# Performance work log

Hardware: AMD Instinct MI355X
Metric: run time of the kernel (lower is better)

Reference implementation:

```python
import jax, jax.numpy as jnp
import numpy as np

B, S, E, H = 2, 2048, 1024, 16
D = E // H
LN_EPS = 1e-5
NORM_EPS = 1e-12  # F.normalize clamp_min


def setup_inputs() -> dict:
    key = jax.random.key(0)
    ks = jax.random.split(key, 4)
    x = jax.random.normal(ks[0], (B, S, E), dtype=jnp.float32)
    qkv_w = jax.random.normal(ks[1], (3 * E, E), dtype=jnp.float32) * 0.02
    qkv_b = jnp.zeros((3 * E,), dtype=jnp.float32)
    out_w = jax.random.normal(ks[2], (E, E), dtype=jnp.float32) * 0.02
    out_b = jnp.zeros((E,), dtype=jnp.float32)
    ln_w = jnp.ones((E,), dtype=jnp.float32)
    ln_b = jnp.zeros((E,), dtype=jnp.float32)
    qknorm_scale = jnp.asarray(E ** -0.5, dtype=jnp.float32)
    # RotaryEmbedding buffer: inv_freq interleaved (emb[::2] = emb[1::2] = base**(-arange(0,E,2)/E))
    base_freq = 10000.0 ** (-(np.arange(0, E, 2).astype(np.float32) / E))
    emb = np.empty((E,), dtype=np.float32)
    emb[::2] = base_freq
    emb[1::2] = base_freq
    inv_freq = jnp.asarray(emb)
    return {"x": x, "ln_w": ln_w, "ln_b": ln_b, "qkv_w": qkv_w, "qkv_b": qkv_b,
            "qknorm_scale": qknorm_scale, "out_w": out_w, "out_b": out_b, "inv_freq": inv_freq}


def _rotate(t, sin, cos):
    # Faithful to source: x1 = even idx (excluding last), x2 = odd idx; cat(-x2, x1)
    x1 = t[..., :-1:2]
    x2 = t[..., 1::2]
    t_rot = jnp.concatenate((-x2, x1), axis=-1)
    return t * cos + t_rot * sin


def _l2norm(t):
    n = jnp.sqrt(jnp.sum(t * t, axis=-1, keepdims=True))
    return t / jnp.maximum(n, NORM_EPS)


def reference(x, ln_w, ln_b, qkv_w, qkv_b, qknorm_scale, out_w, out_b, inv_freq):
    # --- prenorm (LayerNorm, eps=1e-5) ---
    mu = jnp.mean(x, axis=-1, keepdims=True)
    var = jnp.mean((x - mu) ** 2, axis=-1, keepdims=True)
    xn = (x - mu) / jnp.sqrt(var + LN_EPS) * ln_w + ln_b
    # --- QKV projection ---
    qkv = xn @ qkv_w.T + qkv_b  # [B,S,3E]
    q, k, v = jnp.split(qkv, 3, axis=-1)
    # --- rotary (source uses scalar seq*inv_freq, not per-position) ---
    seq = q.shape[1]
    sin = jnp.sin(seq * inv_freq)
    cos = jnp.cos(seq * inv_freq)
    q = _rotate(q, sin, cos)
    k = _rotate(k, sin, cos)
    # --- split heads: [B,S,E] -> [B,H,S,D] ---
    split = lambda t: t.reshape(B, seq, H, D).transpose(0, 2, 1, 3)
    q, k, v = split(q), split(k), split(v)
    # --- qknorm ---
    q = _l2norm(q) * qknorm_scale
    k = _l2norm(k) * qknorm_scale
    # --- scaled dot product with causal mask ---
    aw = jnp.einsum('bhqd,bhkd->bhqk', q, k)  # [B,H,S,S]
    causal = jnp.tril(jnp.ones((seq, seq), dtype=bool))
    aw = jnp.where(causal, aw, jnp.finfo(aw.dtype).min)
    aw = jax.nn.softmax(aw, axis=-1)
    attn = jnp.einsum('bhqk,bhkd->bhqd', aw, v)
    # --- merge heads + out proj ---
    attn = attn.transpose(0, 2, 1, 3).reshape(B, seq, E)
    return attn @ out_w.T + out_b
```

## Files before the change

kernel.cpp:

```cpp
#include <hip/hip_runtime.h>

typedef unsigned short u16;
typedef __attribute__((ext_vector_type(8))) short bf16x8;
typedef __attribute__((ext_vector_type(4))) float f32x4;

#define SS 2048
#define EE 1024
#define HH 16
#define DD 64

__device__ __forceinline__ float b2f(u16 u) {
  union { unsigned int i; float f; } v; v.i = ((unsigned int)u) << 16; return v.f;
}
__device__ __forceinline__ u16 f2b(float f) {
  union { float f; unsigned int i; } v; v.f = f;
  unsigned int i = v.i;
  return (u16)((i + 0x7FFFu + ((i >> 16) & 1u)) >> 16);
}

#define GLD16(g, l)                                                         \
  __builtin_amdgcn_global_load_lds(                                         \
      (const __attribute__((address_space(1))) unsigned int*)(g),           \
      (__attribute__((address_space(3))) unsigned int*)(l), 16, 0, 0)

__global__ __launch_bounds__(256) void k_cvt(const float* __restrict__ src,
                                             u16* __restrict__ dst) {
  const int i = blockIdx.x * 256 + threadIdx.x;
  float4 v = ((const float4*)src)[i];
  ushort4 o;
  o.x = f2b(v.x); o.y = f2b(v.y); o.z = f2b(v.z); o.w = f2b(v.w);
  ((ushort4*)dst)[i] = o;
}

__global__ __launch_bounds__(256) void k_trig(const float* __restrict__ inv_freq,
                                              float2* __restrict__ cs) {
  const int i = blockIdx.x * 256 + threadIdx.x;
  float th = 2048.0f * inv_freq[i];
  cs[i] = make_float2(cosf(th), sinf(th));
}

__global__ __launch_bounds__(256) void k_ln(const float* __restrict__ x,
                                            const float* __restrict__ lw,
                                            const float* __restrict__ lb,
                                            u16* __restrict__ xn) {
  const int row = blockIdx.x, t = threadIdx.x;
  float4 v = ((const float4*)(x + (size_t)row * EE))[t];
  float f0 = v.x, f1 = v.y, f2 = v.z, f3 = v.w;
  float s = f0 + f1 + f2 + f3;
  float ss = f0 * f0 + f1 * f1 + f2 * f2 + f3 * f3;
  for (int o = 1; o < 64; o <<= 1) { s += __shfl_xor(s, o); ss += __shfl_xor(ss, o); }
  __shared__ float red[8];
  int w = t >> 6;
  if ((t & 63) == 0) { red[w] = s; red[4 + w] = ss; }
  __syncthreads();
  s = red[0] + red[1] + red[2] + red[3];
  ss = red[4] + red[5] + red[6] + red[7];
  float mu = s * (1.0f / 1024.0f);
  float var = ss * (1.0f / 1024.0f) - mu * mu;
  float rstd = rsqrtf(var + 1e-5f);
  float4 wv = ((const float4*)lw)[t];
  float4 bv = ((const float4*)lb)[t];
  ushort4 o;
  o.x = f2b((f0 - mu) * rstd * wv.x + bv.x);
  o.y = f2b((f1 - mu) * rstd * wv.y + bv.y);
  o.z = f2b((f2 - mu) * rstd * wv.z + bv.z);
  o.w = f2b((f3 - mu) * rstd * wv.w + bv.w);
  ((ushort4*)(xn + (size_t)row * EE))[t] = o;
}

template <typename OutT>
__device__ __forceinline__ void gemm_body(const u16* __restrict__ A,
                                          const u16* __restrict__ W,
                                          const float* __restrict__ bias,
                                          OutT* __restrict__ C,
                                          int M, int N, int K) {
  __shared__ __align__(16) u16 As[128 * 32];
  __shared__ __align__(16) u16 Ws[128 * 32];
  const int t = threadIdx.x;
  const int m0 = blockIdx.y * 128, n0 = blockIdx.x * 128;
  const int lane = t & 63, w = t >> 6, quad = lane >> 4, l15 = lane & 15;
  const int wm = (w & 1) * 64, wn = (w >> 1) * 64;

  f32x4 zero4 = {0.f, 0.f, 0.f, 0.f};
  f32x4 acc[4][4];
  for (int mi = 0; mi < 4; mi++)
    for (int ni = 0; ni < 4; ni++) acc[mi][ni] = zero4;

  const u16* Ag = A + (size_t)(m0 + (t >> 2)) * K + (t & 3) * 8;
  const u16* Wg = W + (size_t)(n0 + (t >> 2)) * K + (t & 3) * 8;
  const size_t rowskip = (size_t)64 * K;

  for (int k0 = 0; k0 < K; k0 += 32) {
    GLD16(Ag + k0, As + t * 8);
    GLD16(Ag + rowskip + k0, As + 2048 + t * 8);
    GLD16(Wg + k0, Ws + t * 8);
    GLD16(Wg + rowskip + k0, Ws + 2048 + t * 8);
    __syncthreads();
    bf16x8 af[4], wf[4];
#pragma unroll
    for (int i = 0; i < 4; i++) {
      af[i] = *(const bf16x8*)(As + (wm + i * 16 + l15) * 32 + quad * 8);
      wf[i] = *(const bf16x8*)(Ws + (wn + i * 16 + l15) * 32 + quad * 8);
    }
#pragma unroll
    for (int mi = 0; mi < 4; mi++)
#pragma unroll
      for (int ni = 0; ni < 4; ni++)
        acc[mi][ni] = __builtin_amdgcn_mfma_f32_16x16x32_bf16(af[mi], wf[ni], acc[mi][ni], 0, 0, 0);
    __syncthreads();
  }
  for (int mi = 0; mi < 4; mi++)
    for (int ni = 0; ni < 4; ni++) {
      int col = n0 + wn + ni * 16 + l15;
      float bb = bias[col];
      for (int r = 0; r < 4; r++) {
        int grow = m0 + wm + mi * 16 + quad * 4 + r;
        float val = acc[mi][ni][r] + bb;
        if constexpr (sizeof(OutT) == 2) C[(size_t)grow * N + col] = f2b(val);
        else                             C[(size_t)grow * N + col] = val;
      }
    }
}

__global__ __launch_bounds__(256) void k_gemm_b(const u16* A, const u16* W,
                                                const float* bias, u16* C,
                                                int M, int N, int K) {
  gemm_body<u16>(A, W, bias, C, M, N, K);
}
__global__ __launch_bounds__(256) void k_gemm_f(const u16* A, const u16* W,
                                                const float* bias, float* C,
                                                int M, int N, int K) {
  gemm_body<float>(A, W, bias, C, M, N, K);
}

__global__ __launch_bounds__(256) void k_rotnorm(u16* __restrict__ qkv,
                                                 const float2* __restrict__ cs_tab,
                                                 const float* __restrict__ scale_p) {
  __shared__ float qf[1024];
  __shared__ float kf[1024];
  const int row = blockIdx.x, t = threadIdx.x;
  u16* qr = qkv + (size_t)row * 3072;
  u16* kr = qr + 1024;
  ushort4 qv = ((const ushort4*)qr)[t];
  ushort4 kv = ((const ushort4*)kr)[t];
  *(float4*)(qf + 4 * t) = make_float4(b2f(qv.x), b2f(qv.y), b2f(qv.z), b2f(qv.w));
  *(float4*)(kf + 4 * t) = make_float4(b2f(kv.x), b2f(kv.y), b2f(kv.z), b2f(kv.w));
  __syncthreads();
  const float scale = scale_p[0];
  float rq[4], rk[4];
#pragma unroll
  for (int u = 0; u < 4; u++) {
    int j = 4 * t + u;
    float2 cs = cs_tab[j];
    float qrot = (j < 512) ? -qf[2 * j + 1] : qf[2 * (j - 512)];
    float krot = (j < 512) ? -kf[2 * j + 1] : kf[2 * (j - 512)];
    rq[u] = qf[j] * cs.x + qrot * cs.y;
    rk[u] = kf[j] * cs.x + krot * cs.y;
  }
  float ssq = rq[0] * rq[0] + rq[1] * rq[1] + rq[2] * rq[2] + rq[3] * rq[3];
  float ssk = rk[0] * rk[0] + rk[1] * rk[1] + rk[2] * rk[2] + rk[3] * rk[3];
  for (int o = 1; o < 16; o <<= 1) { ssq += __shfl_xor(ssq, o); ssk += __shfl_xor(ssk, o); }
  float qs = scale / fmaxf(sqrtf(ssq), 1e-12f);
  float ks = scale / fmaxf(sqrtf(ssk), 1e-12f);
  ushort4 qo, ko;
  qo.x = f2b(rq[0] * qs); qo.y = f2b(rq[1] * qs); qo.z = f2b(rq[2] * qs); qo.w = f2b(rq[3] * qs);
  ko.x = f2b(rk[0] * ks); ko.y = f2b(rk[1] * ks); ko.z = f2b(rk[2] * ks); ko.w = f2b(rk[3] * ks);
  ((ushort4*)qr)[t] = qo;
  ((ushort4*)kr)[t] = ko;
}

__global__ __launch_bounds__(256) void k_vtrans(const u16* __restrict__ qkv,
                                                u16* __restrict__ vt) {
  __shared__ __align__(16) u16 tile[64 * 72];
  const int st = blockIdx.x, bh = blockIdx.y;
  const int b = bh >> 4, h = bh & 15;
  const int s0 = st * 64, t = threadIdx.x;
  const int si = t >> 2, dc = t & 3;
  const u16* src = qkv + (size_t)(b * SS + s0 + si) * 3072 + 2048 + h * DD;
  bf16x8 v0 = *(const bf16x8*)(src + dc * 8);
  bf16x8 v1 = *(const bf16x8*)(src + (dc + 4) * 8);
#pragma unroll
  for (int u = 0; u < 8; u++) tile[(dc * 8 + u) * 72 + si] = (u16)v0[u];
#pragma unroll
  for (int u = 0; u < 8; u++) tile[((dc + 4) * 8 + u) * 72 + si] = (u16)v1[u];
  __syncthreads();
#pragma unroll
  for (int it = 0; it < 2; it++) {
    int idx = t + it * 256;
    int d = idx >> 3, ch = idx & 7;
    bf16x8 o = *(const bf16x8*)(tile + d * 72 + ch * 8);
    *(bf16x8*)(vt + (size_t)(bh * DD + d) * SS + s0 + ch * 8) = o;
  }
}

__global__ __launch_bounds__(256) void k_attn(const u16* __restrict__ qkv,
                                              const u16* __restrict__ vt,
                                              u16* __restrict__ out) {
  __shared__ __align__(16) u16 Kt[64 * 72];
  __shared__ __align__(16) u16 Vt[64 * 72];
  __shared__ __align__(16) u16 Pt[64 * 72];
  const int bh = blockIdx.y;
  const int b = bh >> 4, h = bh & 15;
  const int t = threadIdx.x, w = t >> 6, lane = t & 63, quad = lane >> 4, l15 = lane & 15;
  const int sr = t >> 2, sc = t & 3;
  const u16* qn = qkv;
  const u16* kn = qkv + 1024;
  f32x4 zero4 = {0.f, 0.f, 0.f, 0.f};

  for (int rep = 0; rep < 2; rep++) {
    const int qt = rep ? 31 - (int)blockIdx.x : (int)blockIdx.x;
    const int q0 = qt * 64;

    bf16x8 qf[2];
    {
      const u16* qrow = qn + (size_t)(b * SS + q0 + 16 * w + l15) * 3072 + h * DD;
      qf[0] = *(const bf16x8*)(qrow + quad * 8);
      qf[1] = *(const bf16x8*)(qrow + 32 + quad * 8);
    }
    f32x4 oacc[4];
    for (int n = 0; n < 4; n++) oacc[n] = zero4;
    float m_i[4] = {-1e30f, -1e30f, -1e30f, -1e30f};
    float l_i[4] = {0.f, 0.f, 0.f, 0.f};

    for (int kt = 0; kt <= qt; kt++) {
      const int k0 = kt * 64;
      const u16* krow = kn + (size_t)(b * SS + k0 + sr) * 3072 + h * DD;
      bf16x8 kv0 = *(const bf16x8*)(krow + sc * 8);
      bf16x8 kv1 = *(const bf16x8*)(krow + (sc + 4) * 8);
      const u16* vrow = vt + (size_t)(bh * DD + sr) * SS + k0;
      bf16x8 vv0 = *(const bf16x8*)(vrow + sc * 8);
      bf16x8 vv1 = *(const bf16x8*)(vrow + (sc + 4) * 8);
      *(bf16x8*)(Kt + sr * 72 + sc * 8) = kv0;
      *(bf16x8*)(Kt + sr * 72 + (sc + 4) * 8) = kv1;
      *(bf16x8*)(Vt + sr * 72 + sc * 8) = vv0;
      *(bf16x8*)(Vt + sr * 72 + (sc + 4) * 8) = vv1;
      __syncthreads();
      f32x4 sacc[4];
#pragma unroll
      for (int n = 0; n < 4; n++) {
        sacc[n] = zero4;
#pragma unroll
        for (int c = 0; c < 2; c++) {
          bf16x8 kfrag = *(const bf16x8*)(Kt + (n * 16 + l15) * 72 + c * 32 + quad * 8);
          sacc[n] = __builtin_amdgcn_mfma_f32_16x16x32_bf16(qf[c], kfrag, sacc[n], 0, 0, 0);
        }
      }
      if (kt == qt) {
#pragma unroll
        for (int n = 0; n < 4; n++)
#pragma unroll
          for (int r = 0; r < 4; r++)
            if (n * 16 + l15 > 16 * w + quad * 4 + r) sacc[n][r] = -1e30f;
      }
#pragma unroll
      for (int r = 0; r < 4; r++) {
        float mx = fmaxf(fmaxf(sacc[0][r], sacc[1][r]), fmaxf(sacc[2][r], sacc[3][r]));
        for (int o = 1; o < 16; o <<= 1) mx = fmaxf(mx, __shfl_xor(mx, o));
        float mn = fmaxf(m_i[r], mx);
        float al = __expf(m_i[r] - mn);
        m_i[r] = mn;
        float rs = 0.f;
#pragma unroll
        for (int n = 0; n < 4; n++) {
          float p = __expf(sacc[n][r] - mn);
          sacc[n][r] = p;
          rs += p;
        }
        for (int o = 1; o < 16; o <<= 1) rs += __shfl_xor(rs, o);
        l_i[r] = al * l_i[r] + rs;
#pragma unroll
        for (int n = 0; n < 4; n++) oacc[n][r] *= al;
      }
#pragma unroll
      for (int n = 0; n < 4; n++)
#pragma unroll
        for (int r = 0; r < 4; r++)
          Pt[(16 * w + quad * 4 + r) * 72 + n * 16 + l15] = f2b(sacc[n][r]);
      __syncthreads();
#pragma unroll
      for (int c = 0; c < 2; c++) {
        bf16x8 pf = *(const bf16x8*)(Pt + (16 * w + l15) * 72 + c * 32 + quad * 8);
#pragma unroll
        for (int n = 0; n < 4; n++) {
          bf16x8 vf = *(const bf16x8*)(Vt + (n * 16 + l15) * 72 + c * 32 + quad * 8);
          oacc[n] = __builtin_amdgcn_mfma_f32_16x16x32_bf16(pf, vf, oacc[n], 0, 0, 0);
        }
      }
      __syncthreads();
    }
    for (int n = 0; n < 4; n++)
      for (int r = 0; r < 4; r++) {
        int row = q0 + 16 * w + quad * 4 + r;
        out[(size_t)(b * SS + row) * EE + h * DD + n * 16 + l15] = f2b(oacc[n][r] / l_i[r]);
      }
  }
}

extern "C" void kernel_launch(void* const* d_in, const int* in_sizes, int n_in,
                              void* d_out, int out_size, void* d_ws, size_t ws_size,
                              hipStream_t stream) {
  const float* x       = (const float*)d_in[0];
  const float* ln_w    = (const float*)d_in[1];
  const float* ln_b    = (const float*)d_in[2];
  const float* qkv_w   = (const float*)d_in[3];
  const float* qkv_b   = (const float*)d_in[4];
  const float* qk_s    = (const float*)d_in[5];
  const float* out_w   = (const float*)d_in[6];
  const float* out_b   = (const float*)d_in[7];
  const float* inv_frq = (const float*)d_in[8];

  u16* ws   = (u16*)d_ws;
  u16* xn   = ws;
  u16* qkv  = ws + (size_t)4096 * 1024;
  u16* wq_b = (u16*)d_out;
  float2* cs_tab = (float2*)((char*)d_out + 6291456);
  u16* vt   = (u16*)d_out + (size_t)4194304;
  u16* wo_b = qkv;

  k_cvt<<<3072, 256, 0, stream>>>(qkv_w, wq_b);
  k_trig<<<4, 256, 0, stream>>>(inv_frq, cs_tab);
  k_ln<<<4096, 256, 0, stream>>>(x, ln_w, ln_b, xn);
  k_gemm_b<<<dim3(24, 32), 256, 0, stream>>>(xn, wq_b, qkv_b, qkv, 4096, 3072, 1024);
  k_rotnorm<<<4096, 256, 0, stream>>>(qkv, cs_tab, qk_s);
  k_vtrans<<<dim3(32, 32), 256, 0, stream>>>(qkv, vt);
  k_attn<<<dim3(16, 32), 256, 0, stream>>>(qkv, vt, xn);
  k_cvt<<<1024, 256, 0, stream>>>(out_w, wo_b);
  k_gemm_f<<<dim3(8, 32), 256, 0, stream>>>(xn, wo_b, out_b, (float*)d_out, 4096, 1024, 1024);
}
```

Measured before the change: 254.9 us.

## Fuse prep kernels, merge rotnorm with V transpose, double-buffer attention, shrink out-proj tile

Merges the weight conversion, trig table and LayerNorm into one launch, and folds the V transpose into the rotary/qknorm kernel, to cut launch count. Attention now double-buffers K/V tiles in shared memory and prefetches the next tile into registers while computing. One barrier per iteration is replaced by a wave-local lgkmcnt wait, because each wave reads back only its own P rows. The output GEMM uses 64-row tiles so it launches twice as many blocks for better occupancy, at the cost of less reuse of W per tile.

```diff
diff --git a/kernel.cpp b/kernel.cpp
--- a/kernel.cpp
+++ b/kernel.cpp
@@ -23,27 +23,30 @@
       (const __attribute__((address_space(1))) unsigned int*)(g),           \
       (__attribute__((address_space(3))) unsigned int*)(l), 16, 0, 0)
 
-__global__ __launch_bounds__(256) void k_cvt(const float* __restrict__ src,
-                                             u16* __restrict__ dst) {
-  const int i = blockIdx.x * 256 + threadIdx.x;
-  float4 v = ((const float4*)src)[i];
-  ushort4 o;
-  o.x = f2b(v.x); o.y = f2b(v.y); o.z = f2b(v.z); o.w = f2b(v.w);
-  ((ushort4*)dst)[i] = o;
-}
-
-__global__ __launch_bounds__(256) void k_trig(const float* __restrict__ inv_freq,
-                                              float2* __restrict__ cs) {
-  const int i = blockIdx.x * 256 + threadIdx.x;
-  float th = 2048.0f * inv_freq[i];
-  cs[i] = make_float2(cosf(th), sinf(th));
-}
-
-__global__ __launch_bounds__(256) void k_ln(const float* __restrict__ x,
-                                            const float* __restrict__ lw,
-                                            const float* __restrict__ lb,
-                                            u16* __restrict__ xn) {
-  const int row = blockIdx.x, t = threadIdx.x;
+__global__ __launch_bounds__(256) void k_prep(const float* __restrict__ qkv_w,
+                                              u16* __restrict__ wq_b,
+                                              const float* __restrict__ inv_freq,
+                                              float2* __restrict__ cs,
+                                              const float* __restrict__ x,
+                                              const float* __restrict__ lw,
+                                              const float* __restrict__ lb,
+                                              u16* __restrict__ xn) {
+  const int bx = blockIdx.x, t = threadIdx.x;
+  if (bx < 3072) {
+    const int i = bx * 256 + t;
+    float4 v = ((const float4*)qkv_w)[i];
+    ushort4 o;
+    o.x = f2b(v.x); o.y = f2b(v.y); o.z = f2b(v.z); o.w = f2b(v.w);
+    ((ushort4*)wq_b)[i] = o;
+    return;
+  }
+  if (bx < 3076) {
+    const int i = (bx - 3072) * 256 + t;
+    float th = 2048.0f * inv_freq[i];
+    cs[i] = make_float2(cosf(th), sinf(th));
+    return;
+  }
+  const int row = bx - 3076;
   float4 v = ((const float4*)(x + (size_t)row * EE))[t];
   float f0 = v.x, f1 = v.y, f2 = v.z, f3 = v.w;
   float s = f0 + f1 + f2 + f3;
@@ -68,22 +71,33 @@
   ((ushort4*)(xn + (size_t)row * EE))[t] = o;
 }
 
-template <typename OutT>
+__global__ __launch_bounds__(256) void k_cvt(const float* __restrict__ src,
+                                             u16* __restrict__ dst) {
+  const int i = blockIdx.x * 256 + threadIdx.x;
+  float4 v = ((const float4*)src)[i];
+  ushort4 o;
+  o.x = f2b(v.x); o.y = f2b(v.y); o.z = f2b(v.z); o.w = f2b(v.w);
+  ((ushort4*)dst)[i] = o;
+}
+
+template <typename OutT, int BM64>
 __device__ __forceinline__ void gemm_body(const u16* __restrict__ A,
                                           const u16* __restrict__ W,
                                           const float* __restrict__ bias,
                                           OutT* __restrict__ C,
                                           int M, int N, int K) {
-  __shared__ __align__(16) u16 As[128 * 32];
+  constexpr int BM = 64 * BM64;
+  constexpr int MI = 2 * BM64;
+  __shared__ __align__(16) u16 As[BM * 32];
   __shared__ __align__(16) u16 Ws[128 * 32];
   const int t = threadIdx.x;
-  const int m0 = blockIdx.y * 128, n0 = blockIdx.x * 128;
+  const int m0 = blockIdx.y * BM, n0 = blockIdx.x * 128;
   const int lane = t & 63, w = t >> 6, quad = lane >> 4, l15 = lane & 15;
-  const int wm = (w & 1) * 64, wn = (w >> 1) * 64;
+  const int wm = (w & 1) * (BM / 2), wn = (w >> 1) * 64;
 
   f32x4 zero4 = {0.f, 0.f, 0.f, 0.f};
-  f32x4 acc[4][4];
-  for (int mi = 0; mi < 4; mi++)
+  f32x4 acc[MI][4];
+  for (int mi = 0; mi < MI; mi++)
     for (int ni = 0; ni < 4; ni++) acc[mi][ni] = zero4;
 
   const u16* Ag = A + (size_t)(m0 + (t >> 2)) * K + (t & 3) * 8;
@@ -92,24 +106,25 @@
 
   for (int k0 = 0; k0 < K; k0 += 32) {
     GLD16(Ag + k0, As + t * 8);
-    GLD16(Ag + rowskip + k0, As + 2048 + t * 8);
+    if constexpr (BM64 == 2) GLD16(Ag + rowskip + k0, As + 2048 + t * 8);
     GLD16(Wg + k0, Ws + t * 8);
     GLD16(Wg + rowskip + k0, Ws + 2048 + t * 8);
     __syncthreads();
-    bf16x8 af[4], wf[4];
-#pragma unroll
-    for (int i = 0; i < 4; i++) {
+    bf16x8 af[MI], wf[4];
+#pragma unroll
+    for (int i = 0; i < MI; i++)
       af[i] = *(const bf16x8*)(As + (wm + i * 16 + l15) * 32 + quad * 8);
+#pragma unroll
+    for (int i = 0; i < 4; i++)
       wf[i] = *(const bf16x8*)(Ws + (wn + i * 16 + l15) * 32 + quad * 8);
-    }
-#pragma unroll
-    for (int mi = 0; mi < 4; mi++)
+#pragma unroll
+    for (int mi = 0; mi < MI; mi++)
 #pragma unroll
       for (int ni = 0; ni < 4; ni++)
         acc[mi][ni] = __builtin_amdgcn_mfma_f32_16x16x32_bf16(af[mi], wf[ni], acc[mi][ni], 0, 0, 0);
     __syncthreads();
   }
-  for (int mi = 0; mi < 4; mi++)
+  for (int mi = 0; mi < MI; mi++)
     for (int ni = 0; ni < 4; ni++) {
       int col = n0 + wn + ni * 16 + l15;
       float bb = bias[col];
@@ -125,57 +140,58 @@
 __global__ __launch_bounds__(256) void k_gemm_b(const u16* A, const u16* W,
                                                 const float* bias, u16* C,
                                                 int M, int N, int K) {
-  gemm_body<u16>(A, W, bias, C, M, N, K);
+  gemm_body<u16, 2>(A, W, bias, C, M, N, K);
 }
 __global__ __launch_bounds__(256) void k_gemm_f(const u16* A, const u16* W,
                                                 const float* bias, float* C,
                                                 int M, int N, int K) {
-  gemm_body<float>(A, W, bias, C, M, N, K);
-}
-
-__global__ __launch_bounds__(256) void k_rotnorm(u16* __restrict__ qkv,
-                                                 const float2* __restrict__ cs_tab,
-                                                 const float* __restrict__ scale_p) {
+  gemm_body<float, 1>(A, W, bias, C, M, N, K);
+}
+
+__global__ __launch_bounds__(256) void k_rotv(u16* __restrict__ qkv,
+                                              const float2* __restrict__ cs_tab,
+                                              const float* __restrict__ scale_p,
+                                              u16* __restrict__ vt) {
   __shared__ float qf[1024];
   __shared__ float kf[1024];
+  __shared__ __align__(16) u16 tile[64 * 72];
   const int row = blockIdx.x, t = threadIdx.x;
-  u16* qr = qkv + (size_t)row * 3072;
-  u16* kr = qr + 1024;
-  ushort4 qv = ((const ushort4*)qr)[t];
-  ushort4 kv = ((const ushort4*)kr)[t];
-  *(float4*)(qf + 4 * t) = make_float4(b2f(qv.x), b2f(qv.y), b2f(qv.z), b2f(qv.w));
-  *(float4*)(kf + 4 * t) = make_float4(b2f(kv.x), b2f(kv.y), b2f(kv.z), b2f(kv.w));
+  {
+    u16* qr = qkv + (size_t)row * 3072;
+    u16* kr = qr + 1024;
+    ushort4 qv = ((const ushort4*)qr)[t];
+    ushort4 kv = ((const ushort4*)kr)[t];
+    *(float4*)(qf + 4 * t) = make_float4(b2f(qv.x), b2f(qv.y), b2f(qv.z), b2f(qv.w));
+    *(float4*)(kf + 4 * t) = make_float4(b2f(kv.x), b2f(kv.y), b2f(kv.z), b2f(kv.w));
+    __syncthreads();
+    const float scale = scale_p[0];
+    float rq[4], rk[4];
+#pragma unroll
+    for (int u = 0; u < 4; u++) {
+      int j = 4 * t + u;
+      float2 cs = cs_tab[j];
+      float qrot = (j < 512) ? -qf[2 * j + 1] : qf[2 * (j - 512)];
+      float krot = (j < 512) ? -kf[2 * j + 1] : kf[2 * (j - 512)];
+      rq[u] = qf[j] * cs.x + qrot * cs.y;
+      rk[u] = kf[j] * cs.x + krot * cs.y;
+    }
+    float ssq = rq[0] * rq[0] + rq[1] * rq[1] + rq[2] * rq[2] + rq[3] * rq[3];
+    float ssk = rk[0] * rk[0] + rk[1] * rk[1] + rk[2] * rk[2] + rk[3] * rk[3];
+    for (int o = 1; o < 16; o <<= 1) { ssq += __shfl_xor(ssq, o); ssk += __shfl_xor(ssk, o); }
+    float qs = scale / fmaxf(sqrtf(ssq), 1e-12f);
+    float ks = scale / fmaxf(sqrtf(ssk), 1e-12f);
+    ushort4 qo, ko;
+    qo.x = f2b(rq[0] * qs); qo.y = f2b(rq[1] * qs); qo.z = f2b(rq[2] * qs); qo.w = f2b(rq[3] * qs);
+    ko.x = f2b(rk[0] * ks); ko.y = f2b(rk[1] * ks); ko.z = f2b(rk[2] * ks); ko.w = f2b(rk[3] * ks);
+    ((ushort4*)qr)[t] = qo;
+    ((ushort4*)kr)[t] = ko;
+  }
+  if (row >= 1024) return;
+  const int st = row & 31, bh = row >> 5;
+  const int b = bh >> 4, h = bh & 15;
+  const int s0 = st * 64;
+  const int si = t >> 2, dc = t & 3;
   __syncthreads();
-  const float scale = scale_p[0];
-  float rq[4], rk[4];
-#pragma unroll
-  for (int u = 0; u < 4; u++) {
-    int j = 4 * t + u;
-    float2 cs = cs_tab[j];
-    float qrot = (j < 512) ? -qf[2 * j + 1] : qf[2 * (j - 512)];
-    float krot = (j < 512) ? -kf[2 * j + 1] : kf[2 * (j - 512)];
-    rq[u] = qf[j] * cs.x + qrot * cs.y;
-    rk[u] = kf[j] * cs.x + krot * cs.y;
-  }
-  float ssq = rq[0] * rq[0] + rq[1] * rq[1] + rq[2] * rq[2] + rq[3] * rq[3];
-  float ssk = rk[0] * rk[0] + rk[1] * rk[1] + rk[2] * rk[2] + rk[3] * rk[3];
-  for (int o = 1; o < 16; o <<= 1) { ssq += __shfl_xor(ssq, o); ssk += __shfl_xor(ssk, o); }
-  float qs = scale / fmaxf(sqrtf(ssq), 1e-12f);
-  float ks = scale / fmaxf(sqrtf(ssk), 1e-12f);
-  ushort4 qo, ko;
-  qo.x = f2b(rq[0] * qs); qo.y = f2b(rq[1] * qs); qo.z = f2b(rq[2] * qs); qo.w = f2b(rq[3] * qs);
-  ko.x = f2b(rk[0] * ks); ko.y = f2b(rk[1] * ks); ko.z = f2b(rk[2] * ks); ko.w = f2b(rk[3] * ks);
-  ((ushort4*)qr)[t] = qo;
-  ((ushort4*)kr)[t] = ko;
-}
-
-__global__ __launch_bounds__(256) void k_vtrans(const u16* __restrict__ qkv,
-                                                u16* __restrict__ vt) {
-  __shared__ __align__(16) u16 tile[64 * 72];
-  const int st = blockIdx.x, bh = blockIdx.y;
-  const int b = bh >> 4, h = bh & 15;
-  const int s0 = st * 64, t = threadIdx.x;
-  const int si = t >> 2, dc = t & 3;
   const u16* src = qkv + (size_t)(b * SS + s0 + si) * 3072 + 2048 + h * DD;
   bf16x8 v0 = *(const bf16x8*)(src + dc * 8);
   bf16x8 v1 = *(const bf16x8*)(src + (dc + 4) * 8);
@@ -196,14 +212,13 @@
 __global__ __launch_bounds__(256) void k_attn(const u16* __restrict__ qkv,
                                               const u16* __restrict__ vt,
                                               u16* __restrict__ out) {
-  __shared__ __align__(16) u16 Kt[64 * 72];
-  __shared__ __align__(16) u16 Vt[64 * 72];
+  __shared__ __align__(16) u16 Kt[2][64 * 72];
+  __shared__ __align__(16) u16 Vt[2][64 * 72];
   __shared__ __align__(16) u16 Pt[64 * 72];
   const int bh = blockIdx.y;
   const int b = bh >> 4, h = bh & 15;
   const int t = threadIdx.x, w = t >> 6, lane = t & 63, quad = lane >> 4, l15 = lane & 15;
   const int sr = t >> 2, sc = t & 3;
-  const u16* qn = qkv;
   const u16* kn = qkv + 1024;
   f32x4 zero4 = {0.f, 0.f, 0.f, 0.f};
 
@@ -213,7 +228,7 @@
 
     bf16x8 qf[2];
     {
-      const u16* qrow = qn + (size_t)(b * SS + q0 + 16 * w + l15) * 3072 + h * DD;
+      const u16* qrow = qkv + (size_t)(b * SS + q0 + 16 * w + l15) * 3072 + h * DD;
       qf[0] = *(const bf16x8*)(qrow + quad * 8);
       qf[1] = *(const bf16x8*)(qrow + 32 + quad * 8);
     }
@@ -222,26 +237,42 @@
     float m_i[4] = {-1e30f, -1e30f, -1e30f, -1e30f};
     float l_i[4] = {0.f, 0.f, 0.f, 0.f};
 
+    bf16x8 kv0, kv1, vv0, vv1;
+    {
+      const u16* krow = kn + (size_t)(b * SS + sr) * 3072 + h * DD;
+      kv0 = *(const bf16x8*)(krow + sc * 8);
+      kv1 = *(const bf16x8*)(krow + (sc + 4) * 8);
+      const u16* vrow = vt + (size_t)(bh * DD + sr) * SS;
+      vv0 = *(const bf16x8*)(vrow + sc * 8);
+      vv1 = *(const bf16x8*)(vrow + (sc + 4) * 8);
+    }
+    __syncthreads();
+    *(bf16x8*)(Kt[0] + sr * 72 + sc * 8) = kv0;
+    *(bf16x8*)(Kt[0] + sr * 72 + (sc + 4) * 8) = kv1;
+    *(bf16x8*)(Vt[0] + sr * 72 + sc * 8) = vv0;
+    *(bf16x8*)(Vt[0] + sr * 72 + (sc + 4) * 8) = vv1;
+    int cur = 0;
+
     for (int kt = 0; kt <= qt; kt++) {
-      const int k0 = kt * 64;
-      const u16* krow = kn + (size_t)(b * SS + k0 + sr) * 3072 + h * DD;
-      bf16x8 kv0 = *(const bf16x8*)(krow + sc * 8);
-      bf16x8 kv1 = *(const bf16x8*)(krow + (sc + 4) * 8);
-      const u16* vrow = vt + (size_t)(bh * DD + sr) * SS + k0;
-      bf16x8 vv0 = *(const bf16x8*)(vrow + sc * 8);
-      bf16x8 vv1 = *(const bf16x8*)(vrow + (sc + 4) * 8);
-      *(bf16x8*)(Kt + sr * 72 + sc * 8) = kv0;
-      *(bf16x8*)(Kt + sr * 72 + (sc + 4) * 8) = kv1;
-      *(bf16x8*)(Vt + sr * 72 + sc * 8) = vv0;
-      *(bf16x8*)(Vt + sr * 72 + (sc + 4) * 8) = vv1;
       __syncthreads();
+      if (kt < qt) {
+        const int k0n = (kt + 1) * 64;
+        const u16* krow = kn + (size_t)(b * SS + k0n + sr) * 3072 + h * DD;
+        kv0 = *(const bf16x8*)(krow + sc * 8);
+        kv1 = *(const bf16x8*)(krow + (sc + 4) * 8);
+        const u16* vrow = vt + (size_t)(bh * DD + sr) * SS + k0n;
+        vv0 = *(const bf16x8*)(vrow + sc * 8);
+        vv1 = *(const bf16x8*)(vrow + (sc + 4) * 8);
+      }
+      const u16* Kc = Kt[cur];
+      const u16* Vc = Vt[cur];
       f32x4 sacc[4];
 #pragma unroll
       for (int n = 0; n < 4; n++) {
         sacc[n] = zero4;
 #pragma unroll
         for (int c = 0; c < 2; c++) {
-          bf16x8 kfrag = *(const bf16x8*)(Kt + (n * 16 + l15) * 72 + c * 32 + quad * 8);
+          bf16x8 kfrag = *(const bf16x8*)(Kc + (n * 16 + l15) * 72 + c * 32 + quad * 8);
           sacc[n] = __builtin_amdgcn_mfma_f32_16x16x32_bf16(qf[c], kfrag, sacc[n], 0, 0, 0);
         }
       }
@@ -276,17 +307,25 @@
 #pragma unroll
         for (int r = 0; r < 4; r++)
           Pt[(16 * w + quad * 4 + r) * 72 + n * 16 + l15] = f2b(sacc[n][r]);
-      __syncthreads();
+      asm volatile("s_waitcnt lgkmcnt(0)" ::: "memory");
 #pragma unroll
       for (int c = 0; c < 2; c++) {
         bf16x8 pf = *(const bf16x8*)(Pt + (16 * w + l15) * 72 + c * 32 + quad * 8);
 #pragma unroll
         for (int n = 0; n < 4; n++) {
-          bf16x8 vf = *(const bf16x8*)(Vt + (n * 16 + l15) * 72 + c * 32 + quad * 8);
+          bf16x8 vf = *(const bf16x8*)(Vc + (n * 16 + l15) * 72 + c * 32 + quad * 8);
           oacc[n] = __builtin_amdgcn_mfma_f32_16x16x32_bf16(pf, vf, oacc[n], 0, 0, 0);
         }
       }
-      __syncthreads();
+      if (kt < qt) {
+        u16* Kn2 = Kt[cur ^ 1];
+        u16* Vn2 = Vt[cur ^ 1];
+        *(bf16x8*)(Kn2 + sr * 72 + sc * 8) = kv0;
+        *(bf16x8*)(Kn2 + sr * 72 + (sc + 4) * 8) = kv1;
+        *(bf16x8*)(Vn2 + sr * 72 + sc * 8) = vv0;
+        *(bf16x8*)(Vn2 + sr * 72 + (sc + 4) * 8) = vv1;
+      }
+      cur ^= 1;
     }
     for (int n = 0; n < 4; n++)
       for (int r = 0; r < 4; r++) {
@@ -317,13 +356,10 @@
   u16* vt   = (u16*)d_out + (size_t)4194304;
   u16* wo_b = qkv;
 
-  k_cvt<<<3072, 256, 0, stream>>>(qkv_w, wq_b);
-  k_trig<<<4, 256, 0, stream>>>(inv_frq, cs_tab);
-  k_ln<<<4096, 256, 0, stream>>>(x, ln_w, ln_b, xn);
+  k_prep<<<7172, 256, 0, stream>>>(qkv_w, wq_b, inv_frq, cs_tab, x, ln_w, ln_b, xn);
   k_gemm_b<<<dim3(24, 32), 256, 0, stream>>>(xn, wq_b, qkv_b, qkv, 4096, 3072, 1024);
-  k_rotnorm<<<4096, 256, 0, stream>>>(qkv, cs_tab, qk_s);
-  k_vtrans<<<dim3(32, 32), 256, 0, stream>>>(qkv, vt);
+  k_rotv<<<4096, 256, 0, stream>>>(qkv, cs_tab, qk_s, vt);
   k_attn<<<dim3(16, 32), 256, 0, stream>>>(qkv, vt, xn);
   k_cvt<<<1024, 256, 0, stream>>>(out_w, wo_b);
-  k_gemm_f<<<dim3(8, 32), 256, 0, stream>>>(xn, wo_b, out_b, (float*)d_out, 4096, 1024, 1024);
-}
+  k_gemm_f<<<dim3(8, 64), 256, 0, stream>>>(xn, wo_b, out_b, (float*)d_out, 4096, 1024, 1024);
+}
```

Result: faster. 239.5 us (-6.0%).
